# Performance work log

Hardware: AMD Instinct MI355X
Metric: run time of the kernel (lower is better)

Reference implementation:

```python
import jax, jax.numpy as jnp
import numpy as np

ALPHA = 0.7
L_CHAMFER, L_EDGE, L_SMOOTH, L_NORMAL = 1.0, 2.0, 1.0, 0.5
EPS = 1e-8

N, M, P, G, F = 8192, 8192, 8192, 8192, 16384


def _cdist(a, b):
    # Euclidean distance matrix, (N,3) x (M,3) -> (N,M); matches torch.cdist
    d2 = (jnp.sum(a * a, axis=1)[:, None]
          + jnp.sum(b * b, axis=1)[None, :]
          - 2.0 * a @ b.T)
    return jnp.sqrt(jnp.maximum(d2, 0.0))


def _chamfer(a, b):
    d = _cdist(a, b)
    return (d.min(axis=1).mean() + d.min(axis=0).mean()) * 0.5


def _unit(x, key):
    v = jax.random.normal(key, x, dtype=jnp.float32)
    return v / jnp.linalg.norm(v, axis=1, keepdims=True)


def setup_inputs() -> dict:
    key = jax.random.key(0)
    ks = jax.random.split(key, 7)
    return {
        "student_verts": jax.random.normal(ks[0], (N, 3), dtype=jnp.float32),
        "student_normals": _unit((N, 3), ks[1]),
        "teacher_verts": jax.random.normal(ks[2], (M, 3), dtype=jnp.float32),
        "teacher_normals": _unit((M, 3), ks[3]),
        "teacher_points": jax.random.normal(ks[4], (P, 3), dtype=jnp.float32),
        "gt_points": jax.random.normal(ks[5], (G, 3), dtype=jnp.float32),
        "faces": jax.random.randint(ks[6], (F, 3), 0, N, dtype=jnp.int32),
    }


def reference(student_verts, student_normals, teacher_verts, teacher_normals,
              teacher_points, gt_points, faces):
    # --- chamfer losses ---
    loss_teacher = _chamfer(student_verts, teacher_points)
    loss_gt = _chamfer(student_verts, gt_points)
    loss_chamfer = ALPHA * loss_teacher + (1.0 - ALPHA) * loss_gt

    # --- mesh edge loss: mean squared edge length ---
    edges = jnp.concatenate([faces[:, [0, 1]], faces[:, [1, 2]], faces[:, [2, 0]]], axis=0)  # (3F,2)
    ev = student_verts[edges[:, 0]] - student_verts[edges[:, 1]]
    loss_edge = jnp.sum(ev * ev, axis=1).mean()

    # --- uniform laplacian smoothing: mean || mean(nbrs) - v || ---
    nverts = student_verts.shape[0]
    src = jnp.concatenate([edges[:, 0], edges[:, 1]])
    dst = jnp.concatenate([edges[:, 1], edges[:, 0]])
    nbr_sum = jax.ops.segment_sum(student_verts[dst], src, num_segments=nverts)
    deg = jax.ops.segment_sum(jnp.ones_like(src, dtype=jnp.float32), src, num_segments=nverts)
    lap = nbr_sum / jnp.maximum(deg, 1.0)[:, None] - student_verts
    loss_smooth = jnp.linalg.norm(lap, axis=1).mean()
    # replicate norm with safe sqrt for grad stability

    # --- normal loss via nearest teacher vertex ---
    d_tv = _cdist(student_verts, teacher_verts)  # (N,M)
    nearest_idx = jnp.argmin(d_tv, axis=1)
    target_normals = teacher_normals[nearest_idx]  # (N,3)
    num = jnp.sum(student_normals * target_normals, axis=1)
    den = (jnp.maximum(jnp.linalg.norm(student_normals, axis=1), EPS)
           * jnp.maximum(jnp.linalg.norm(target_normals, axis=1), EPS))
    loss_normal = 1.0 - (num / den).mean()

    total = (L_CHAMFER * loss_chamfer + L_EDGE * loss_edge
             + L_SMOOTH * loss_smooth + L_NORMAL * loss_normal)
    return total
```

## Files before the change

### kernel.cpp

```cpp
#include <hip/hip_runtime.h>


typedef short sh8 __attribute__((ext_vector_type(8)));
typedef float f32x16 __attribute__((ext_vector_type(16)));

#define BLK 256
#define TR 2
#define JTILES 64

__device__ __forceinline__ float wave_reduce_sum(float v) {
#pragma unroll
  for (int o = 32; o > 0; o >>= 1) v += __shfl_down(v, o, 64);
  return v;
}

__device__ __forceinline__ unsigned flipf(float f) {
  unsigned b = __float_as_uint(f);
  return (b & 0x80000000u) ? ~b : (b | 0x80000000u);
}
__device__ __forceinline__ float unflipf(unsigned u) {
  unsigned b = (u & 0x80000000u) ? (u ^ 0x80000000u) : ~u;
  return __uint_as_float(b);
}

__device__ __forceinline__ unsigned short f2bf(float x) {
  unsigned u = __float_as_uint(x);
  unsigned r = (u + 0x7FFFu + ((u >> 16) & 1u)) >> 16;
  return (unsigned short)r;
}
__device__ __forceinline__ float bf2f(unsigned short b) {
  return __uint_as_float(((unsigned)b) << 16);
}

__device__ void pack_pt(int i, float x, float y, float z, sh8* Ap, sh8* Bp) {
  float aa = fmaf(x, x, fmaf(y, y, z * z));
  unsigned short hx = f2bf(x), hy = f2bf(y), hz = f2bf(z);
  float lx = x - bf2f(hx), ly = y - bf2f(hy), lz = z - bf2f(hz);
  unsigned short haa = f2bf(aa);
  float laa = aa - bf2f(haa);
  const short ONE = (short)0x3F80;
  const int base = (i >> 5) * 64 + (i & 31);
  if (Ap) {
    unsigned short nhx = f2bf(-2.f * bf2f(hx)), nhy = f2bf(-2.f * bf2f(hy)),
                   nhz = f2bf(-2.f * bf2f(hz));
    unsigned short nlx = f2bf(-2.f * lx), nly = f2bf(-2.f * ly),
                   nlz = f2bf(-2.f * lz);
    sh8 lo, hi;
    lo[0] = (short)nhx; lo[1] = (short)nhy; lo[2] = (short)nhz;
    lo[3] = (short)nlx; lo[4] = (short)nly; lo[5] = (short)nlz;
    lo[6] = (short)nhx; lo[7] = (short)nhy;
    hi[0] = (short)nhz; hi[1] = (short)haa; hi[2] = (short)f2bf(laa);
    hi[3] = ONE; hi[4] = ONE; hi[5] = 0; hi[6] = 0; hi[7] = 0;
    Ap[base] = lo; Ap[base + 32] = hi;
  }
  {
    unsigned short lxb = f2bf(lx), lyb = f2bf(ly), lzb = f2bf(lz);
    sh8 lo, hi;
    lo[0] = (short)hx; lo[1] = (short)hy; lo[2] = (short)hz;
    lo[3] = (short)hx; lo[4] = (short)hy; lo[5] = (short)hz;
    lo[6] = (short)lxb; lo[7] = (short)lyb;
    hi[0] = (short)lzb; hi[1] = ONE; hi[2] = ONE;
    hi[3] = (short)haa; hi[4] = (short)f2bf(laa);
    hi[5] = 0; hi[6] = 0; hi[7] = 0;
    Bp[base] = lo; Bp[base + 32] = hi;
  }
}

struct Packs {
  sh8 *Asv, *Atp, *Agp;
  sh8 *Bsv, *Btp, *Bgp, *Btv;
};

__global__ void init_ws_kernel(Packs pk,
                               const float* __restrict__ sv,
                               const float* __restrict__ tp,
                               const float* __restrict__ gp,
                               const float* __restrict__ tv,
                               unsigned long long* __restrict__ min64, int n64,
                               unsigned* __restrict__ minbits, int nmin,
                               float* __restrict__ zr, int nz, int n) {
  const int stride = gridDim.x * blockDim.x;
  const int t0 = blockIdx.x * blockDim.x + threadIdx.x;
  for (int i = t0; i < n64; i += stride) min64[i] = ~0ull;
  for (int i = t0; i < nmin; i += stride) minbits[i] = 0xFF800000u;
  for (int i = t0; i < nz; i += stride) zr[i] = 0.0f;
  for (int i = t0; i < n; i += stride) {
    pack_pt(i, sv[3 * i], sv[3 * i + 1], sv[3 * i + 2], pk.Asv, pk.Bsv);
    pack_pt(i, tp[3 * i], tp[3 * i + 1], tp[3 * i + 2], pk.Atp, pk.Btp);
    pack_pt(i, gp[3 * i], gp[3 * i + 1], gp[3 * i + 2], pk.Agp, pk.Bgp);
    pack_pt(i, tv[3 * i], tv[3 * i + 1], tv[3 * i + 2], (sh8*)0, pk.Btv);
  }
}

struct Desc {
  const sh8* Ap[5];
  const sh8* Bp[5];
  void* out[5];
  const int* fc; int f;
  const float* sv;
  float* nbr; float* deg; float* acc;
};

__global__ void __launch_bounds__(BLK) mega_kernel(Desc d) {
  const int pass = blockIdx.z;
  const int t = threadIdx.x;

  if (pass == 5) {
    const int nE = 3 * d.f;
    const int bid = blockIdx.y * gridDim.x + blockIdx.x;
    const int stride = gridDim.x * gridDim.y * BLK;
    float es = 0.f;
    for (int e = bid * BLK + t; e < nE; e += stride) {
      int a, b;
      if (e < d.f)          { a = d.fc[3 * e + 0];  b = d.fc[3 * e + 1]; }
      else if (e < 2 * d.f) { int q = e - d.f;     a = d.fc[3 * q + 1]; b = d.fc[3 * q + 2]; }
      else                  { int q = e - 2 * d.f; a = d.fc[3 * q + 2]; b = d.fc[3 * q + 0]; }
      float ax = d.sv[3 * a], ay = d.sv[3 * a + 1], az = d.sv[3 * a + 2];
      float bx = d.sv[3 * b], by = d.sv[3 * b + 1], bz = d.sv[3 * b + 2];
      float dx = ax - bx, dy = ay - by, dz = az - bz;
      es += fmaf(dx, dx, fmaf(dy, dy, dz * dz));
      atomicAdd(&d.nbr[3 * a + 0], bx);
      atomicAdd(&d.nbr[3 * a + 1], by);
      atomicAdd(&d.nbr[3 * a + 2], bz);
      atomicAdd(&d.nbr[3 * b + 0], ax);
      atomicAdd(&d.nbr[3 * b + 1], ay);
      atomicAdd(&d.nbr[3 * b + 2], az);
      atomicAdd(&d.deg[a], 1.0f);
      atomicAdd(&d.deg[b], 1.0f);
    }
    es = wave_reduce_sum(es);
    if ((t & 63) == 0) atomicAdd(&d.acc[4], es);
    return;
  }

  const int wave = t >> 6, lane = t & 63;
  const int jt0 = blockIdx.y * JTILES;
  const float INF = __int_as_float(0x7f800000);
  f32x16 zc;
#pragma unroll
  for (int q = 0; q < 16; ++q) zc[q] = 0.f;

  const sh8* __restrict__ Ap = d.Ap[pass];
  const sh8* __restrict__ Bp = d.Bp[pass];

  if (pass < 4) {
    if (blockIdx.x >= 32) return;
    const int rt0 = (blockIdx.x * 4 + wave) * TR;
    sh8 af0 = Ap[rt0 * 64 + lane];
    sh8 af1 = Ap[(rt0 + 1) * 64 + lane];
    f32x16 r0, r1;
#pragma unroll
    for (int q = 0; q < 16; ++q) { r0[q] = INF; r1[q] = INF; }
#pragma unroll 2
    for (int jt = 0; jt < JTILES; ++jt) {
      sh8 bf = Bp[(jt0 + jt) * 64 + lane];
      f32x16 c0 = __builtin_amdgcn_mfma_f32_32x32x16_bf16(af0, bf, zc, 0, 0, 0);
      f32x16 c1 = __builtin_amdgcn_mfma_f32_32x32x16_bf16(af1, bf, zc, 0, 0, 0);
      r0 = __builtin_elementwise_min(r0, c0);
      r1 = __builtin_elementwise_min(r1, c1);
    }
    unsigned* __restrict__ out = (unsigned*)d.out[pass];
#pragma unroll
    for (int a = 0; a < TR; ++a) {
#pragma unroll
      for (int q = 0; q < 16; ++q) {
        float v = (a == 0) ? r0[q] : r1[q];
        v = fminf(v, __shfl_xor(v, 1));
        v = fminf(v, __shfl_xor(v, 2));
        v = fminf(v, __shfl_xor(v, 4));
        v = fminf(v, __shfl_xor(v, 8));
        v = fminf(v, __shfl_xor(v, 16));
        if ((lane & 31) == 0) {
          int row = (rt0 + a) * 32 + (q & 3) + 8 * (q >> 2) + 4 * (lane >> 5);
          atomicMin(out + row, flipf(v));
        }
      }
    }
  } else {
    const int rt = blockIdx.x * 4 + wave;
    sh8 af = Ap[rt * 64 + lane];
    f32x16 m;
    float idx[16];
#pragma unroll
    for (int q = 0; q < 16; ++q) { m[q] = INF; idx[q] = 0.f; }
#pragma unroll 2
    for (int jt = 0; jt < JTILES; ++jt) {
      sh8 bf = Bp[(jt0 + jt) * 64 + lane];
      f32x16 c = __builtin_amdgcn_mfma_f32_32x32x16_bf16(af, bf, zc, 0, 0, 0);
      float colf = (float)((jt0 + jt) * 32 + (lane & 31));
#pragma unroll
      for (int q = 0; q < 16; ++q) {
        bool cm = c[q] < m[q];
        m[q] = cm ? c[q] : m[q];
        idx[q] = cm ? colf : idx[q];
      }
    }
    unsigned long long* __restrict__ out = (unsigned long long*)d.out[4];
#pragma unroll
    for (int q = 0; q < 16; ++q) {
      float v = m[q], ix = idx[q];
#pragma unroll
      for (int s = 0; s < 5; ++s) {
        int msk = 1 << s;
        float ov = __shfl_xor(v, msk);
        float oi = __shfl_xor(ix, msk);
        bool take = (ov < v) || (ov == v && oi < ix);
        v = take ? ov : v;
        ix = take ? oi : ix;
      }
      if ((lane & 31) == 0) {
        int row = rt * 32 + (q & 3) + 8 * (q >> 2) + 4 * (lane >> 5);
        unsigned long long packed =
            ((unsigned long long)flipf(v) << 32) | (unsigned)(int)ix;
        atomicMin(out + row, packed);
      }
    }
  }
}

__global__ void __launch_bounds__(BLK) post_kernel(
    const float* __restrict__ sv, const float* __restrict__ sn,
    const float* __restrict__ tn,
    const float* __restrict__ nbr, const float* __restrict__ deg,
    const unsigned* __restrict__ minbase,
    const unsigned long long* __restrict__ min64,
    int n, int p, int g, int f, float* __restrict__ acc,
    int* __restrict__ cnt, float* __restrict__ out) {
  const int task = blockIdx.y;
  const int i = blockIdx.x * blockDim.x + threadIdx.x;
  float s = 0.f;
  int accIdx;
  if (task == 0) {
    accIdx = 5;
    if (i < n) {
      float dd = fmaxf(deg[i], 1.0f);
      float lx = nbr[3 * i + 0] / dd - sv[3 * i + 0];
      float ly = nbr[3 * i + 1] / dd - sv[3 * i + 1];
      float lz = nbr[3 * i + 2] / dd - sv[3 * i + 2];
      s = sqrtf(fmaf(lx, lx, fmaf(ly, ly, lz * lz)));
    }
  } else if (task == 1) {
    accIdx = 6;
    if (i < n) {
      int idx = (int)(min64[i] & 0xffffffffull);
      float sx = sn[3 * i], sy = sn[3 * i + 1], sz = sn[3 * i + 2];
      float tx = tn[3 * idx], ty = tn[3 * idx + 1], tz = tn[3 * idx + 2];
      float num = fmaf(sx, tx, fmaf(sy, ty, sz * tz));
      float ns = sqrtf(fmaf(sx, sx, fmaf(sy, sy, sz * sz)));
      float nt = sqrtf(fmaf(tx, tx, fmaf(ty, ty, tz * tz)));
      s = num / (fmaxf(ns, 1e-8f) * fmaxf(nt, 1e-8f));
    }
  } else {
    const int seg = task - 2;
    accIdx = seg;
    const int off = (seg == 0) ? 0 : (seg == 1) ? n : (seg == 2) ? (n + p) : (2 * n + p);
    const int cntN = (seg == 1) ? p : n;
    if (i < cntN) {
      float d2 = unflipf(minbase[off + i]);
      s = sqrtf(fmaxf(d2, 0.0f));
    }
  }
  s = wave_reduce_sum(s);
  if ((threadIdx.x & 63) == 0) atomicAdd(&acc[accIdx], s);

  __syncthreads();
  __threadfence();
  __shared__ int last;
  if (threadIdx.x == 0)
    last = (atomicAdd(cnt, 1) == (int)(gridDim.x * gridDim.y) - 1);
  __syncthreads();
  if (last && threadIdx.x == 0) {
    float a[7];
#pragma unroll
    for (int q = 0; q < 7; ++q) a[q] = atomicAdd(&acc[q], 0.0f);
    float lt = 0.5f * (a[0] / (float)n + a[1] / (float)p);
    float lg = 0.5f * (a[2] / (float)n + a[3] / (float)g);
    float chamfer = 0.7f * lt + 0.3f * lg;
    float edge = a[4] / (float)(3 * f);
    float smooth = a[5] / (float)n;
    float normal = 1.0f - a[6] / (float)n;
    out[0] = chamfer + 2.0f * edge + smooth + 0.5f * normal;
  }
}

extern "C" void kernel_launch(void* const* d_in, const int* in_sizes, int n_in,
                              void* d_out, int out_size, void* d_ws, size_t ws_size,
                              hipStream_t stream) {
  const float* sv = (const float*)d_in[0];
  const float* sn = (const float*)d_in[1];
  const float* tv = (const float*)d_in[2];
  const float* tn = (const float*)d_in[3];
  const float* tp = (const float*)d_in[4];
  const float* gp = (const float*)d_in[5];
  const int*   fc = (const int*)d_in[6];
  const int n = in_sizes[0] / 3;
  const int m = in_sizes[2] / 3;
  const int p = in_sizes[4] / 3;
  const int g = in_sizes[5] / 3;
  const int f = in_sizes[6] / 3;

  char* w = (char*)d_ws;
  Packs pk;
  pk.Asv = (sh8*)w; w += (size_t)n * 32;
  pk.Atp = (sh8*)w; w += (size_t)p * 32;
  pk.Agp = (sh8*)w; w += (size_t)g * 32;
  pk.Bsv = (sh8*)w; w += (size_t)n * 32;
  pk.Btp = (sh8*)w; w += (size_t)p * 32;
  pk.Bgp = (sh8*)w; w += (size_t)g * 32;
  pk.Btv = (sh8*)w; w += (size_t)m * 32;
  unsigned long long* min64 = (unsigned long long*)w; w += (size_t)n * 8;
  unsigned* minbase = (unsigned*)w; w += (size_t)(n + p + n + g) * 4;
  float* nbr = (float*)w; w += (size_t)n * 3 * 4;
  float* deg = (float*)w; w += (size_t)n * 4;
  float* acc = (float*)w; w += 8 * 4;
  int* cnt = (int*)w;

  unsigned* minA_tp = minbase;
  unsigned* minB_tp = minA_tp + n;
  unsigned* minA_gt = minB_tp + p;
  unsigned* minB_gt = minA_gt + n;

  const int nmin = n + p + n + g;
  const int nz = n * 3 + n + 8 + 1;

  init_ws_kernel<<<64, BLK, 0, stream>>>(pk, sv, tp, gp, tv,
                                         min64, n, minbase, nmin, nbr, nz, n);

  Desc d;
  d.Ap[0] = pk.Asv; d.Bp[0] = pk.Btp; d.out[0] = minA_tp;
  d.Ap[1] = pk.Atp; d.Bp[1] = pk.Bsv; d.out[1] = minB_tp;
  d.Ap[2] = pk.Asv; d.Bp[2] = pk.Bgp; d.out[2] = minA_gt;
  d.Ap[3] = pk.Agp; d.Bp[3] = pk.Bsv; d.out[3] = minB_gt;
  d.Ap[4] = pk.Asv; d.Bp[4] = pk.Btv; d.out[4] = min64;
  d.fc = fc; d.f = f; d.sv = sv;
  d.nbr = nbr; d.deg = deg; d.acc = acc;

  dim3 pgrid(64, 4, 6);
  mega_kernel<<<pgrid, BLK, 0, stream>>>(d);

  dim3 tgrid((n + BLK - 1) / BLK, 6);
  post_kernel<<<tgrid, BLK, 0, stream>>>(sv, sn, tn, nbr, deg,
                                         minbase, min64, n, p, g, f,
                                         acc, cnt, (float*)d_out);
}
```

Before: 138.2 us.

## Fuse symmetric chamfer passes: derive column minima from same MFMA tiles

Instead of computing the A-to-B and B-to-A distance matrices in separate passes, each chamfer block now computes one tile and reduces it both along rows (as before) and along columns through shared-memory atomics that are flushed to global memory at the end. This halves the MFMA work and the packing for the two chamfer pairs, and the transposed packs are no longer built. The grid is flattened to 1D with 16-tile column chunks, a one-ahead B prefetch, and launch_bounds occupancy 8. The cost is extra per-tile column reductions, LDS atomics and more global atomics per block, and each block has less work to amortize its setup.

```diff
diff --git a/kernel.cpp b/kernel.cpp
--- a/kernel.cpp
+++ b/kernel.cpp
@@ -5,8 +5,12 @@
 typedef float f32x16 __attribute__((ext_vector_type(16)));
 
 #define BLK 256
-#define TR 2
-#define JTILES 64
+#define CCT 16
+#define NCC 16
+#define NRB 64
+#define NB_F (2 * NRB * NCC)
+#define NB_A (NRB * NCC)
+#define NB_E 64
 
 __device__ __forceinline__ float wave_reduce_sum(float v) {
 #pragma unroll
@@ -53,7 +57,7 @@
     hi[3] = ONE; hi[4] = ONE; hi[5] = 0; hi[6] = 0; hi[7] = 0;
     Ap[base] = lo; Ap[base + 32] = hi;
   }
-  {
+  if (Bp) {
     unsigned short lxb = f2bf(lx), lyb = f2bf(ly), lzb = f2bf(lz);
     sh8 lo, hi;
     lo[0] = (short)hx; lo[1] = (short)hy; lo[2] = (short)hz;
@@ -66,12 +70,8 @@
   }
 }
 
-struct Packs {
-  sh8 *Asv, *Atp, *Agp;
-  sh8 *Bsv, *Btp, *Bgp, *Btv;
-};
-
-__global__ void init_ws_kernel(Packs pk,
+__global__ void init_ws_kernel(sh8* __restrict__ Asv, sh8* __restrict__ Btp,
+                               sh8* __restrict__ Bgp, sh8* __restrict__ Btv,
                                const float* __restrict__ sv,
                                const float* __restrict__ tp,
                                const float* __restrict__ gp,
@@ -85,32 +85,33 @@
   for (int i = t0; i < nmin; i += stride) minbits[i] = 0xFF800000u;
   for (int i = t0; i < nz; i += stride) zr[i] = 0.0f;
   for (int i = t0; i < n; i += stride) {
-    pack_pt(i, sv[3 * i], sv[3 * i + 1], sv[3 * i + 2], pk.Asv, pk.Bsv);
-    pack_pt(i, tp[3 * i], tp[3 * i + 1], tp[3 * i + 2], pk.Atp, pk.Btp);
-    pack_pt(i, gp[3 * i], gp[3 * i + 1], gp[3 * i + 2], pk.Agp, pk.Bgp);
-    pack_pt(i, tv[3 * i], tv[3 * i + 1], tv[3 * i + 2], (sh8*)0, pk.Btv);
+    pack_pt(i, sv[3 * i], sv[3 * i + 1], sv[3 * i + 2], Asv, (sh8*)0);
+    pack_pt(i, tp[3 * i], tp[3 * i + 1], tp[3 * i + 2], (sh8*)0, Btp);
+    pack_pt(i, gp[3 * i], gp[3 * i + 1], gp[3 * i + 2], (sh8*)0, Bgp);
+    pack_pt(i, tv[3 * i], tv[3 * i + 1], tv[3 * i + 2], (sh8*)0, Btv);
   }
 }
 
 struct Desc {
-  const sh8* Ap[5];
-  const sh8* Bp[5];
-  void* out[5];
+  const sh8 *Asv, *Btp, *Bgp, *Btv;
+  unsigned *minA_tp, *minB_tp, *minA_gt, *minB_gt;
+  unsigned long long* min64;
   const int* fc; int f;
   const float* sv;
   float* nbr; float* deg; float* acc;
 };
 
-__global__ void __launch_bounds__(BLK) mega_kernel(Desc d) {
-  const int pass = blockIdx.z;
+__global__ void __launch_bounds__(BLK, 8) mega_kernel(Desc d) {
   const int t = threadIdx.x;
-
-  if (pass == 5) {
+  const int bid = blockIdx.x;
+  const int wave = t >> 6, lane = t & 63;
+  const float INF = __int_as_float(0x7f800000);
+
+  if (bid >= NB_F + NB_A) {
     const int nE = 3 * d.f;
-    const int bid = blockIdx.y * gridDim.x + blockIdx.x;
-    const int stride = gridDim.x * gridDim.y * BLK;
+    const int stride = NB_E * BLK;
     float es = 0.f;
-    for (int e = bid * BLK + t; e < nE; e += stride) {
+    for (int e = (bid - NB_F - NB_A) * BLK + t; e < nE; e += stride) {
       int a, b;
       if (e < d.f)          { a = d.fc[3 * e + 0];  b = d.fc[3 * e + 1]; }
       else if (e < 2 * d.f) { int q = e - d.f;     a = d.fc[3 * q + 1]; b = d.fc[3 * q + 2]; }
@@ -133,59 +134,77 @@
     return;
   }
 
-  const int wave = t >> 6, lane = t & 63;
-  const int jt0 = blockIdx.y * JTILES;
-  const float INF = __int_as_float(0x7f800000);
   f32x16 zc;
 #pragma unroll
   for (int q = 0; q < 16; ++q) zc[q] = 0.f;
 
-  const sh8* __restrict__ Ap = d.Ap[pass];
-  const sh8* __restrict__ Bp = d.Bp[pass];
-
-  if (pass < 4) {
-    if (blockIdx.x >= 32) return;
-    const int rt0 = (blockIdx.x * 4 + wave) * TR;
-    sh8 af0 = Ap[rt0 * 64 + lane];
-    sh8 af1 = Ap[(rt0 + 1) * 64 + lane];
-    f32x16 r0, r1;
-#pragma unroll
-    for (int q = 0; q < 16; ++q) { r0[q] = INF; r1[q] = INF; }
-#pragma unroll 2
-    for (int jt = 0; jt < JTILES; ++jt) {
-      sh8 bf = Bp[(jt0 + jt) * 64 + lane];
-      f32x16 c0 = __builtin_amdgcn_mfma_f32_32x32x16_bf16(af0, bf, zc, 0, 0, 0);
-      f32x16 c1 = __builtin_amdgcn_mfma_f32_32x32x16_bf16(af1, bf, zc, 0, 0, 0);
-      r0 = __builtin_elementwise_min(r0, c0);
-      r1 = __builtin_elementwise_min(r1, c1);
-    }
-    unsigned* __restrict__ out = (unsigned*)d.out[pass];
-#pragma unroll
-    for (int a = 0; a < TR; ++a) {
-#pragma unroll
-      for (int q = 0; q < 16; ++q) {
-        float v = (a == 0) ? r0[q] : r1[q];
-        v = fminf(v, __shfl_xor(v, 1));
-        v = fminf(v, __shfl_xor(v, 2));
-        v = fminf(v, __shfl_xor(v, 4));
-        v = fminf(v, __shfl_xor(v, 8));
-        v = fminf(v, __shfl_xor(v, 16));
-        if ((lane & 31) == 0) {
-          int row = (rt0 + a) * 32 + (q & 3) + 8 * (q >> 2) + 4 * (lane >> 5);
-          atomicMin(out + row, flipf(v));
-        }
+  if (bid < NB_F) {
+    __shared__ unsigned colmin[CCT * 32];
+    const int fsel = bid >> 10;
+    const int rem = bid & 1023;
+    const int rb = rem >> 4, cc = rem & 15;
+    const sh8* __restrict__ Ap = d.Asv;
+    const sh8* __restrict__ Bp = fsel ? d.Bgp : d.Btp;
+    unsigned* __restrict__ outR = fsel ? d.minA_gt : d.minA_tp;
+    unsigned* __restrict__ outC = fsel ? d.minB_gt : d.minB_tp;
+
+    for (int i = t; i < CCT * 32; i += BLK) colmin[i] = 0xFFFFFFFFu;
+    __syncthreads();
+
+    const int rt = rb * 4 + wave;
+    sh8 af = Ap[(size_t)rt * 64 + lane];
+    const int jt0 = cc * CCT;
+    sh8 bf = Bp[(size_t)jt0 * 64 + lane];
+    f32x16 r;
+#pragma unroll
+    for (int q = 0; q < 16; ++q) r[q] = INF;
+
+#pragma unroll 4
+    for (int jt = 0; jt < CCT; ++jt) {
+      int jn = (jt + 1 < CCT) ? (jt + 1) : jt;
+      sh8 bfn = Bp[(size_t)(jt0 + jn) * 64 + lane];
+      f32x16 c = __builtin_amdgcn_mfma_f32_32x32x16_bf16(af, bf, zc, 0, 0, 0);
+      r = __builtin_elementwise_min(r, c);
+      float cv = c[0];
+#pragma unroll
+      for (int q = 1; q < 16; ++q) cv = fminf(cv, c[q]);
+      cv = fminf(cv, __shfl_xor(cv, 32));
+      if (lane < 32) atomicMin(&colmin[(jt << 5) | lane], flipf(cv));
+      bf = bfn;
+    }
+
+    unsigned* __restrict__ outRow = outR;
+#pragma unroll
+    for (int q = 0; q < 16; ++q) {
+      float v = r[q];
+      v = fminf(v, __shfl_xor(v, 1));
+      v = fminf(v, __shfl_xor(v, 2));
+      v = fminf(v, __shfl_xor(v, 4));
+      v = fminf(v, __shfl_xor(v, 8));
+      v = fminf(v, __shfl_xor(v, 16));
+      if ((lane & 31) == 0) {
+        int row = rt * 32 + (q & 3) + 8 * (q >> 2) + 4 * (lane >> 5);
+        atomicMin(outRow + row, flipf(v));
       }
     }
+    __syncthreads();
+    for (int i = t; i < CCT * 32; i += BLK)
+      atomicMin(outC + cc * (CCT * 32) + i, colmin[i]);
   } else {
-    const int rt = blockIdx.x * 4 + wave;
-    sh8 af = Ap[rt * 64 + lane];
+    const int rem = bid - NB_F;
+    const int rb = rem >> 4, cc = rem & 15;
+    const int rt = rb * 4 + wave;
+    const sh8* __restrict__ Ap = d.Asv;
+    const sh8* __restrict__ Bp = d.Btv;
+    sh8 af = Ap[(size_t)rt * 64 + lane];
+    const int jt0 = cc * CCT;
     f32x16 m;
     float idx[16];
 #pragma unroll
     for (int q = 0; q < 16; ++q) { m[q] = INF; idx[q] = 0.f; }
 #pragma unroll 2
-    for (int jt = 0; jt < JTILES; ++jt) {
-      sh8 bf = Bp[(jt0 + jt) * 64 + lane];
+    for (int jt = 0; jt < CCT; ++jt) {
+      sh8 bf = Bp[(size_t)(jt0 + jt) * 64 + lane];
       f32x16 c = __builtin_amdgcn_mfma_f32_32x32x16_bf16(af, bf, zc, 0, 0, 0);
       float colf = (float)((jt0 + jt) * 32 + (lane & 31));
 #pragma unroll
@@ -195,7 +214,7 @@
         idx[q] = cm ? colf : idx[q];
       }
     }
-    unsigned long long* __restrict__ out = (unsigned long long*)d.out[4];
+    unsigned long long* __restrict__ out = d.min64;
 #pragma unroll
     for (int q = 0; q < 16; ++q) {
       float v = m[q], ix = idx[q];
@@ -300,14 +319,10 @@
   const int f = in_sizes[6] / 3;
 
   char* w = (char*)d_ws;
-  Packs pk;
-  pk.Asv = (sh8*)w; w += (size_t)n * 32;
-  pk.Atp = (sh8*)w; w += (size_t)p * 32;
-  pk.Agp = (sh8*)w; w += (size_t)g * 32;
-  pk.Bsv = (sh8*)w; w += (size_t)n * 32;
-  pk.Btp = (sh8*)w; w += (size_t)p * 32;
-  pk.Bgp = (sh8*)w; w += (size_t)g * 32;
-  pk.Btv = (sh8*)w; w += (size_t)m * 32;
+  sh8* Asv = (sh8*)w; w += (size_t)n * 32;
+  sh8* Btp = (sh8*)w; w += (size_t)p * 32;
+  sh8* Bgp = (sh8*)w; w += (size_t)g * 32;
+  sh8* Btv = (sh8*)w; w += (size_t)m * 32;
   unsigned long long* min64 = (unsigned long long*)w; w += (size_t)n * 8;
   unsigned* minbase = (unsigned*)w; w += (size_t)(n + p + n + g) * 4;
   float* nbr = (float*)w; w += (size_t)n * 3 * 4;
@@ -315,28 +330,23 @@
   float* acc = (float*)w; w += 8 * 4;
   int* cnt = (int*)w;
 
-  unsigned* minA_tp = minbase;
-  unsigned* minB_tp = minA_tp + n;
-  unsigned* minA_gt = minB_tp + p;
-  unsigned* minB_gt = minA_gt + n;
-
   const int nmin = n + p + n + g;
   const int nz = n * 3 + n + 8 + 1;
 
-  init_ws_kernel<<<64, BLK, 0, stream>>>(pk, sv, tp, gp, tv,
+  init_ws_kernel<<<64, BLK, 0, stream>>>(Asv, Btp, Bgp, Btv, sv, tp, gp, tv,
                                          min64, n, minbase, nmin, nbr, nz, n);
 
   Desc d;
-  d.Ap[0] = pk.Asv; d.Bp[0] = pk.Btp; d.out[0] = minA_tp;
-  d.Ap[1] = pk.Atp; d.Bp[1] = pk.Bsv; d.out[1] = minB_tp;
-  d.Ap[2] = pk.Asv; d.Bp[2] = pk.Bgp; d.out[2] = minA_gt;
-  d.Ap[3] = pk.Agp; d.Bp[3] = pk.Bsv; d.out[3] = minB_gt;
-  d.Ap[4] = pk.Asv; d.Bp[4] = pk.Btv; d.out[4] = min64;
+  d.Asv = Asv; d.Btp = Btp; d.Bgp = Bgp; d.Btv = Btv;
+  d.minA_tp = minbase;
+  d.minB_tp = minbase + n;
+  d.minA_gt = minbase + n + p;
+  d.minB_gt = minbase + 2 * n + p;
+  d.min64 = min64;
   d.fc = fc; d.f = f; d.sv = sv;
   d.nbr = nbr; d.deg = deg; d.acc = acc;
 
-  dim3 pgrid(64, 4, 6);
-  mega_kernel<<<pgrid, BLK, 0, stream>>>(d);
+  mega_kernel<<<NB_F + NB_A + NB_E, BLK, 0, stream>>>(d);
 
   dim3 tgrid((n + BLK - 1) / BLK, 6);
   post_kernel<<<tgrid, BLK, 0, stream>>>(sv, sn, tn, nbr, deg,
```

Result: slower. 250.3 us (+81.2%).
